# Performance work log

Hardware: AMD Instinct MI355X
Metric: run time of the kernel (lower is better)

Reference implementation:

```python
import jax, jax.numpy as jnp
import numpy as np

# Winograd F(2x2, 3x3) transform matrices
B = jnp.array([[1.0, 0.0, 0.0, 0.0],
               [0.0, 1.0, -1.0, 1.0],
               [-1.0, 1.0, 1.0, 0.0],
               [0.0, 0.0, 0.0, -1.0]], dtype=jnp.float32)
G = jnp.array([[1.0, 0.0, 0.0],
               [0.5, 0.5, 0.5],
               [0.5, -0.5, 0.5],
               [0.0, 0.0, 1.0]], dtype=jnp.float32)
A = jnp.array([[1.0, 0.0],
               [1.0, 1.0],
               [1.0, -1.0],
               [0.0, -1.0]], dtype=jnp.float32)

PADDING = 1


def setup_inputs() -> dict:
    key = jax.random.key(0)
    k1, k2 = jax.random.split(key)
    x = jax.random.normal(k1, (16, 128, 56, 56), dtype=jnp.float32)
    kernel = jax.random.normal(k2, (128, 128, 3, 3), dtype=jnp.float32) * 0.05
    return {"x": x, "kernel": kernel}


def _winograd_fwd(x, kernel):
    # Pad input
    x = jnp.pad(x, ((0, 0), (0, 0), (PADDING, PADDING), (PADDING, PADDING)))
    N, C, H, W = x.shape
    a, overlap, m = 4, 2, 2  # tile size, stride, output tile
    Th = (H - a) // overlap + 1
    Tw = (W - a) // overlap + 1
    H_out, W_out = H - 2, W - 2

    # Filter transform: U = G @ g @ G^T  -> (K, C, 4, 4)
    U = jnp.einsum('ij,kcjl,ml->kcim', G, kernel, G)

    # Extract overlapping 4x4 tiles with stride 2: (N, C, Th, Tw, 4, 4)
    ii = (jnp.arange(Th) * overlap)[:, None] + jnp.arange(a)[None, :]  # (Th, 4)
    jj = (jnp.arange(Tw) * overlap)[:, None] + jnp.arange(a)[None, :]  # (Tw, 4)
    d = x[:, :, ii]               # (N, C, Th, 4, W)
    d = d[:, :, :, :, jj]         # (N, C, Th, 4, Tw, 4)
    d = d.transpose(0, 1, 2, 4, 3, 5)  # (N, C, Th, Tw, 4, 4)

    # Input transform: V = B^T @ d @ B
    V = jnp.einsum('ji,nchwjk,kl->nchwil', B, d, B)  # (N, C, Th, Tw, 4, 4)

    # Elementwise multiply + channel reduction: (N, K, Th, Tw, 4, 4)
    M = jnp.einsum('kcij,nchwij->nkhwij', U, V)

    # Output transform: Y_tile = A^T @ M @ A -> (N, K, Th, Tw, 2, 2)
    Yt = jnp.einsum('ji,nkhwjl,lm->nkhwim', A, M, A)

    # Reassemble tiles into (N, K, H_out, W_out)
    Y = Yt.transpose(0, 1, 2, 4, 3, 5).reshape(N, Yt.shape[1], H_out, W_out)
    return Y


def reference(x, kernel):
    return _winograd_fwd(x, kernel)
```

## Files before the change

### kernel.cpp

```cpp
#include <hip/hip_runtime.h>
#include <hip/hip_bf16.h>

typedef __attribute__((ext_vector_type(8))) short bf16x8;
typedef __attribute__((ext_vector_type(16))) float f32x16;

#define CC 128
#define KK 128
#define HH 56
#define WW 56
#define HW (HH * WW)

#define WT_OFF 0
#define XP_OFF (512 * 1024)

__device__ __forceinline__ unsigned short f2bf(float f) {
  unsigned int u = __builtin_bit_cast(unsigned int, f);
  u += 0x7FFFu + ((u >> 16) & 1u);
  return (unsigned short)(u >> 16);
}

__device__ __forceinline__ void gload_lds16(const void* g, void* l) {
  __builtin_amdgcn_global_load_lds((__attribute__((address_space(1))) void*)g,
                                   (__attribute__((address_space(3))) void*)l,
                                   16, 0, 0);
}

__global__ void wtrans_kernel(const float* __restrict__ kin,
                              unsigned short* __restrict__ wt2) {
  int idx = blockIdx.x * 256 + threadIdx.x;
  int j = idx & 7;
  int l = (idx >> 3) & 63;
  int kf = (idx >> 9) & 3;
  int cs = (idx >> 11) & 3;
  int m = idx >> 13;
  int ch = (m >= 9) ? 1 : 0;
  int rs = m - ch * 9;
  int k = kf * 32 + (l & 31);
  int c = ch * 64 + cs * 16 + (l >> 5) * 8 + j;
  wt2[idx] = f2bf(kin[(k * CC + c) * 9 + rs]);
}

__global__ void prepack_kernel(const float* __restrict__ x,
                               unsigned short* __restrict__ xp) {
  int idx = blockIdx.x * 256 + threadIdx.x;
  int w = idx & 63;
  int r = idx >> 6;
  int h = r % 58;
  int t = r / 58;
  bool ok = (w >= 1) && (w <= 56) && (h >= 1) && (h <= 56);
  const float* src = x + (size_t)t * 8 * HW + (h - 1) * WW + (w - 1);
  unsigned short o[8];
#pragma unroll
  for (int ci = 0; ci < 8; ++ci) {
    float v = ok ? src[ci * HW] : 0.f;
    o[ci] = f2bf(v);
  }
  *(bf16x8*)(xp + (size_t)idx * 8) = *(bf16x8*)o;
}

__global__ __launch_bounds__(512, 2) void conv_kernel(
    const unsigned short* __restrict__ xp, const unsigned short* __restrict__ wt2,
    float* __restrict__ out) {
  __shared__ __align__(16) unsigned char xs[2 * 6 * 64 * 128];

  const int tid = threadIdx.x;
  const int lane = tid & 63;
  const int wv = tid >> 6;
  const int bh = blockIdx.x;
  const int n = blockIdx.y;
  const int r0 = bh * 4;

  const int p = lane & 31;
  const int dr = p >> 3;
  const int dw = p & 7;
  const int hi = lane >> 5;

  const int kp = wv >> 2;
  const int sh = wv & 3;
  const int ns = (sh == 3) ? 1 : 2;
  const int s0 = sh * 2;

  {
    const int oct = (lane & 7) ^ ((lane >> 3) & 7);
    const int col = wv * 8 + (lane >> 3);
    const unsigned short* g0 =
        xp + ((((size_t)n * 16 + oct) * 58 + r0) * 64 + col) * 8;
#pragma unroll
    for (int ch = 0; ch < 2; ++ch) {
#pragma unroll
      for (int lr = 0; lr < 6; ++lr) {
        gload_lds16(g0 + ch * (8 * 58 * 64 * 8) + lr * 512,
                    xs + ch * 49152 + lr * 8192 + wv * 1024);
      }
    }
  }

  f32x16 acc[2][2] = {};
  bf16x8 A0[8], A1[8];

  auto ldA = [&](int step, bf16x8* D) {
#pragma unroll
    for (int cs = 0; cs < 4; ++cs)
#pragma unroll
      for (int kfl = 0; kfl < 2; ++kfl)
        D[cs * 2 + kfl] = *(const bf16x8*)(
            wt2 + (((step * 4 + cs) * 4 + kp * 2 + kfl) << 9) + lane * 8);
  };

  asm volatile("s_waitcnt vmcnt(6)" ::: "memory");
  __builtin_amdgcn_s_barrier();
  asm volatile("" ::: "memory");

  ldA(0, A0);

  auto phase = [&](const int ch, const unsigned char* buf) {
#pragma unroll
    for (int rs = 0; rs < 9; ++rs) {
      const int step = ch * 9 + rs;
      bf16x8* Ac = (step & 1) ? A1 : A0;
      bf16x8* An = (step & 1) ? A0 : A1;
      if (step < 17) ldA(step + 1, An);
      const int fr = (rs * 11) >> 5;
      const int fs = rs - fr * 3;
      const int rbase = ((dr + fr) * 64 + dw + fs) << 7;
      const int xr = (dw + fs) & 7;
#pragma unroll
      for (int cs = 0; cs < 4; ++cs) {
        const int sb = rbase + ((((cs << 1) + hi) ^ xr) << 4);
#pragma unroll
        for (int si = 0; si < 2; ++si) {
          if (si < ns) {
            bf16x8 b = *(const bf16x8*)(buf + sb + (s0 + si) * 1024);
            acc[0][si] = __builtin_amdgcn_mfma_f32_32x32x16_bf16(
                Ac[cs * 2 + 0], b, acc[0][si], 0, 0, 0);
            acc[1][si] = __builtin_amdgcn_mfma_f32_32x32x16_bf16(
                Ac[cs * 2 + 1], b, acc[1][si], 0, 0, 0);
          }
        }
      }
    }
  };

  phase(0, xs);
  __syncthreads();
  phase(1, xs + 49152);

#pragma unroll
  for (int kfl = 0; kfl < 2; ++kfl) {
#pragma unroll
    for (int si = 0; si < 2; ++si) {
      if (si < ns) {
        const int s = s0 + si;
#pragma unroll
        for (int r = 0; r < 16; ++r) {
          const int krow =
              kp * 64 + kfl * 32 + (r & 3) + ((r >> 2) << 3) + (hi << 2);
          out[(((size_t)n * KK + krow) * HH + (r0 + dr)) * WW + s * 8 + dw] =
              acc[kfl][si][r];
        }
      }
    }
  }
}

extern "C" void kernel_launch(void* const* d_in, const int* in_sizes, int n_in,
                              void* d_out, int out_size, void* d_ws, size_t ws_size,
                              hipStream_t stream) {
  const float* x = (const float*)d_in[0];
  const float* kin = (const float*)d_in[1];
  float* out = (float*)d_out;
  unsigned short* wt2 = (unsigned short*)((char*)d_ws + WT_OFF);
  unsigned short* xp = (unsigned short*)((char*)d_ws + XP_OFF);

  hipLaunchKernelGGL(prepack_kernel, dim3(3712), dim3(256), 0, stream, x, xp);
  hipLaunchKernelGGL(wtrans_kernel, dim3(576), dim3(256), 0, stream, kin, wt2);
  hipLaunchKernelGGL(conv_kernel, dim3(14, 16), dim3(512), 0, stream, xp, wt2, out);
}
```

Baseline: 37.70 us.

## Retile conv into 4x16 spatial tiles with 16x16 MFMA and split-K reduction

The conv kernel now tiles output as 4 rows by 16 columns per block (56x16 grid of 256-thread blocks instead of 14x16 of 512). Each wave uses 16x16x32 bf16 MFMAs over 64 output channels and half of the input channels, and the two channel halves are summed through LDS at the end. Weights are re-laid out to match, and both A and B fragments are double-buffered in registers across the 18 (rs, ks) steps. The aim is more blocks for occupancy and a smaller LDS footprint per block. The costs are a split-K reduction through LDS and extra halo reloads, including wasted columns in the last width tile.

```diff
diff --git a/kernel.cpp b/kernel.cpp
--- a/kernel.cpp
+++ b/kernel.cpp
@@ -2,7 +2,7 @@
 #include <hip/hip_bf16.h>
 
 typedef __attribute__((ext_vector_type(8))) short bf16x8;
-typedef __attribute__((ext_vector_type(16))) float f32x16;
+typedef __attribute__((ext_vector_type(4))) float f32x4;
 
 #define CC 128
 #define KK 128
@@ -10,7 +10,6 @@
 #define WW 56
 #define HW (HH * WW)
 
-#define WT_OFF 0
 #define XP_OFF (512 * 1024)
 
 __device__ __forceinline__ unsigned short f2bf(float f) {
@@ -23,21 +22,6 @@
   __builtin_amdgcn_global_load_lds((__attribute__((address_space(1))) void*)g,
                                    (__attribute__((address_space(3))) void*)l,
                                    16, 0, 0);
-}
-
-__global__ void wtrans_kernel(const float* __restrict__ kin,
-                              unsigned short* __restrict__ wt2) {
-  int idx = blockIdx.x * 256 + threadIdx.x;
-  int j = idx & 7;
-  int l = (idx >> 3) & 63;
-  int kf = (idx >> 9) & 3;
-  int cs = (idx >> 11) & 3;
-  int m = idx >> 13;
-  int ch = (m >= 9) ? 1 : 0;
-  int rs = m - ch * 9;
-  int k = kf * 32 + (l & 31);
-  int c = ch * 64 + cs * 16 + (l >> 5) * 8 + j;
-  wt2[idx] = f2bf(kin[(k * CC + c) * 9 + rs]);
 }
 
 __global__ void prepack_kernel(const float* __restrict__ x,
@@ -58,105 +42,121 @@
   *(bf16x8*)(xp + (size_t)idx * 8) = *(bf16x8*)o;
 }
 
-__global__ __launch_bounds__(512, 2) void conv_kernel(
-    const unsigned short* __restrict__ xp, const unsigned short* __restrict__ wt2,
+__global__ void wtrans_kernel(const float* __restrict__ kin,
+                              unsigned short* __restrict__ wt6) {
+  int e = blockIdx.x * 256 + threadIdx.x;
+  int j = e & 7;
+  int l = (e >> 3) & 63;
+  int f = (e >> 9) & 3;
+  int kp = (e >> 11) & 1;
+  int ks = (e >> 12) & 1;
+  int cp = (e >> 13) & 1;
+  int rs = e >> 14;
+  int k = kp * 64 + f * 16 + (l & 15);
+  int c = cp * 64 + ks * 32 + (l >> 4) * 8 + j;
+  wt6[e] = f2bf(kin[(k * CC + c) * 9 + rs]);
+}
+
+__global__ __launch_bounds__(256, 3) void conv_kernel(
+    const unsigned short* __restrict__ xp, const unsigned short* __restrict__ wt6,
     float* __restrict__ out) {
-  __shared__ __align__(16) unsigned char xs[2 * 6 * 64 * 128];
+  __shared__ __align__(16) unsigned char xs[32768];
 
   const int tid = threadIdx.x;
   const int lane = tid & 63;
   const int wv = tid >> 6;
-  const int bh = blockIdx.x;
+  const int bx = blockIdx.x;
+  const int bh = bx >> 2;
+  const int bw = bx & 3;
   const int n = blockIdx.y;
   const int r0 = bh * 4;
+  const int w0 = bw * 16;
 
-  const int p = lane & 31;
-  const int dr = p >> 3;
-  const int dw = p & 7;
-  const int hi = lane >> 5;
+  const int cidx = lane & 15;
+  const int q = lane >> 4;
 
-  const int kp = wv >> 2;
-  const int sh = wv & 3;
-  const int ns = (sh == 3) ? 1 : 2;
-  const int s0 = sh * 2;
+  const int kp = wv >> 1;
+  const int cp = wv & 1;
+  const int obase = cp * 8 + q;
 
-  {
-    const int oct = (lane & 7) ^ ((lane >> 3) & 7);
-    const int col = wv * 8 + (lane >> 3);
-    const unsigned short* g0 =
-        xp + ((((size_t)n * 16 + oct) * 58 + r0) * 64 + col) * 8;
 #pragma unroll
-    for (int ch = 0; ch < 2; ++ch) {
-#pragma unroll
-      for (int lr = 0; lr < 6; ++lr) {
-        gload_lds16(g0 + ch * (8 * 58 * 64 * 8) + lr * 512,
-                    xs + ch * 49152 + lr * 8192 + wv * 1024);
-      }
+  for (int t = 0; t < 7; ++t) {
+    const int i = wv + 4 * t;
+    if (i < 27) {
+      const int L = i * 64 + lane;
+      const int s = L & 15;
+      const int cell = L >> 4;
+      const int col = cell % 18;
+      const int row = cell / 18;
+      const int o = (s - col) & 15;
+      const unsigned short* src =
+          xp + ((((size_t)(n * 16 + o)) * 58 + (r0 + row)) * 64 + (w0 + col)) * 8;
+      gload_lds16(src, xs + i * 1024);
     }
   }
+  asm volatile("s_waitcnt vmcnt(0)" ::: "memory");
+  __syncthreads();
 
-  f32x16 acc[2][2] = {};
-  bf16x8 A0[8], A1[8];
+  f32x4 acc[4][4] = {};
+  bf16x8 Ar[2][4], Br[2][4];
 
-  auto ldA = [&](int step, bf16x8* D) {
+  auto ldA = [&](int rs, int ks, bf16x8* D) {
+    const unsigned short* base =
+        wt6 + (((((rs * 2 + cp) * 2 + ks) * 2 + kp) * 4) << 9) + lane * 8;
 #pragma unroll
-    for (int cs = 0; cs < 4; ++cs)
+    for (int f = 0; f < 4; ++f) D[f] = *(const bf16x8*)(base + f * 512);
+  };
+  auto ldB = [&](int fr, int fs, int ks, bf16x8* D) {
+    const int colp = cidx + fs;
+    const int slot = (obase + ks * 4 + colp) & 15;
 #pragma unroll
-      for (int kfl = 0; kfl < 2; ++kfl)
-        D[cs * 2 + kfl] = *(const bf16x8*)(
-            wt2 + (((step * 4 + cs) * 4 + kp * 2 + kfl) << 9) + lane * 8);
+    for (int fi = 0; fi < 4; ++fi)
+      D[fi] = *(const bf16x8*)(xs + ((fi + fr) * 18 + colp) * 256 + slot * 16);
   };
 
-  asm volatile("s_waitcnt vmcnt(6)" ::: "memory");
-  __builtin_amdgcn_s_barrier();
-  asm volatile("" ::: "memory");
-
-  ldA(0, A0);
-
-  auto phase = [&](const int ch, const unsigned char* buf) {
-#pragma unroll
-    for (int rs = 0; rs < 9; ++rs) {
-      const int step = ch * 9 + rs;
-      bf16x8* Ac = (step & 1) ? A1 : A0;
-      bf16x8* An = (step & 1) ? A0 : A1;
-      if (step < 17) ldA(step + 1, An);
-      const int fr = (rs * 11) >> 5;
-      const int fs = rs - fr * 3;
-      const int rbase = ((dr + fr) * 64 + dw + fs) << 7;
-      const int xr = (dw + fs) & 7;
-#pragma unroll
-      for (int cs = 0; cs < 4; ++cs) {
-        const int sb = rbase + ((((cs << 1) + hi) ^ xr) << 4);
-#pragma unroll
-        for (int si = 0; si < 2; ++si) {
-          if (si < ns) {
-            bf16x8 b = *(const bf16x8*)(buf + sb + (s0 + si) * 1024);
-            acc[0][si] = __builtin_amdgcn_mfma_f32_32x32x16_bf16(
-                Ac[cs * 2 + 0], b, acc[0][si], 0, 0, 0);
-            acc[1][si] = __builtin_amdgcn_mfma_f32_32x32x16_bf16(
-                Ac[cs * 2 + 1], b, acc[1][si], 0, 0, 0);
-          }
-        }
-      }
-    }
-  };
-
-  phase(0, xs);
-  __syncthreads();
-  phase(1, xs + 49152);
+  ldA(0, 0, Ar[0]);
+  ldB(0, 0, 0, Br[0]);
 
 #pragma unroll
-  for (int kfl = 0; kfl < 2; ++kfl) {
+  for (int u = 0; u < 18; ++u) {
+    const int rsn = (u + 1) >> 1;
+    const int ksn = (u + 1) & 1;
+    if (u < 17) {
+      ldA(rsn, ksn, Ar[(u + 1) & 1]);
+      ldB(rsn / 3, rsn % 3, ksn, Br[(u + 1) & 1]);
+    }
 #pragma unroll
-    for (int si = 0; si < 2; ++si) {
-      if (si < ns) {
-        const int s = s0 + si;
+    for (int f = 0; f < 4; ++f)
 #pragma unroll
-        for (int r = 0; r < 16; ++r) {
-          const int krow =
-              kp * 64 + kfl * 32 + (r & 3) + ((r >> 2) << 3) + (hi << 2);
-          out[(((size_t)n * KK + krow) * HH + (r0 + dr)) * WW + s * 8 + dw] =
-              acc[kfl][si][r];
+      for (int fi = 0; fi < 4; ++fi)
+        acc[f][fi] = __builtin_amdgcn_mfma_f32_16x16x32_bf16(
+            Ar[u & 1][f], Br[u & 1][fi], acc[f][fi], 0, 0, 0);
+  }
+
+  __syncthreads();
+  if (cp == 1) {
+#pragma unroll
+    for (int f = 0; f < 4; ++f)
+#pragma unroll
+      for (int fi = 0; fi < 4; ++fi)
+        *(f32x4*)(xs + kp * 16384 + ((f * 4 + fi) * 64 + lane) * 16) = acc[f][fi];
+  }
+  __syncthreads();
+  if (cp == 0) {
+    const bool wok = (bw < 3) || (cidx < 8);
+#pragma unroll
+    for (int f = 0; f < 4; ++f) {
+#pragma unroll
+      for (int fi = 0; fi < 4; ++fi) {
+        f32x4 other = *(const f32x4*)(xs + kp * 16384 + ((f * 4 + fi) * 64 + lane) * 16);
+        f32x4 r = acc[f][fi] + other;
+        if (wok) {
+          const int k = kp * 64 + f * 16 + q * 4;
+          float* op = out + (((size_t)n * KK + k) * HH + (r0 + fi)) * WW + w0 + cidx;
+          op[0 * HW] = r[0];
+          op[1 * HW] = r[1];
+          op[2 * HW] = r[2];
+          op[3 * HW] = r[3];
         }
       }
     }
@@ -169,10 +169,10 @@
   const float* x = (const float*)d_in[0];
   const float* kin = (const float*)d_in[1];
   float* out = (float*)d_out;
-  unsigned short* wt2 = (unsigned short*)((char*)d_ws + WT_OFF);
+  unsigned short* wt6 = (unsigned short*)d_ws;
   unsigned short* xp = (unsigned short*)((char*)d_ws + XP_OFF);
 
   hipLaunchKernelGGL(prepack_kernel, dim3(3712), dim3(256), 0, stream, x, xp);
-  hipLaunchKernelGGL(wtrans_kernel, dim3(576), dim3(256), 0, stream, kin, wt2);
-  hipLaunchKernelGGL(conv_kernel, dim3(14, 16), dim3(512), 0, stream, xp, wt2, out);
+  hipLaunchKernelGGL(wtrans_kernel, dim3(576), dim3(256), 0, stream, kin, wt6);
+  hipLaunchKernelGGL(conv_kernel, dim3(56, 16), dim3(256), 0, stream, xp, wt6, out);
 }
```

Measured after the change: 63.35 us. +68.0%, slower.
